# Kernel optimization log

Hardware: AMD Instinct MI355X
Metric: run time of the kernel (lower is better)

The kernel has to match this reference:

```python
import jax, jax.numpy as jnp
import numpy as np

N_NODES = 25000
N_EDGES = 250000
DIM = 64
HEADS = 4
BN_EPS = 1e-5


def setup_inputs() -> dict:
    key = jax.random.key(0)
    ks = jax.random.split(key, 6)
    x = jax.random.normal(ks[0], (N_NODES, DIM), dtype=jnp.float32)
    edge_index = jax.random.randint(ks[1], (2, N_EDGES), 0, N_NODES)
    edge_attr = jax.random.normal(ks[2], (N_EDGES, DIM), dtype=jnp.float32)
    # learned params of GATGNN_AGAT_LAYER (xavier-ish scale)
    W = jax.random.normal(ks[3], (2 * DIM, HEADS * DIM), dtype=jnp.float32) * 0.05
    att = jax.random.normal(ks[4], (1, HEADS, 2 * DIM), dtype=jnp.float32) * 0.05
    bias = jnp.zeros((DIM,), dtype=jnp.float32)
    # BatchNorm1d(heads) in eval mode (running stats)
    bn_gamma = jnp.ones((HEADS,), dtype=jnp.float32)
    bn_beta = jnp.zeros((HEADS,), dtype=jnp.float32)
    bn_mean = jnp.zeros((HEADS,), dtype=jnp.float32)
    bn_var = jnp.ones((HEADS,), dtype=jnp.float32)
    return {"x": x, "edge_attr": edge_attr, "W": W, "att": att, "bias": bias,
            "bn_gamma": bn_gamma, "bn_beta": bn_beta, "bn_mean": bn_mean,
            "bn_var": bn_var, "edge_index": edge_index}


def reference(x, edge_attr, W, att, bias, bn_gamma, bn_beta, bn_mean, bn_var, edge_index):
    act = jax.nn.softplus  # act='softplus' in DSDCrystal
    # flow='target_to_source': i = edge_index[0] (aggregation index), j = edge_index[1]
    idx_i = edge_index[0]
    idx_j = edge_index[1]
    x_i = x[idx_i]                                   # [E, D] gather
    x_j = x[idx_j]                                   # [E, D] gather
    out_i = act(jnp.concatenate([x_i, edge_attr], axis=-1) @ W)  # [E, H*D]
    out_j = act(jnp.concatenate([x_j, edge_attr], axis=-1) @ W)  # [E, H*D]
    out_i = out_i.reshape(-1, HEADS, DIM)            # [E, H, D]
    out_j = out_j.reshape(-1, HEADS, DIM)
    # multi-head attention logits
    alpha = act(jnp.sum(jnp.concatenate([out_i, out_j], axis=-1) * att, axis=-1))  # [E, H]
    # BatchNorm1d(heads), eval mode
    alpha = act((alpha - bn_mean) / jnp.sqrt(bn_var + BN_EPS) * bn_gamma + bn_beta)
    # segment softmax over edges sharing the same target node i
    amax = jax.ops.segment_max(alpha, idx_i, num_segments=N_NODES)  # [N, H]
    e = jnp.exp(alpha - amax[idx_i])
    denom = jax.ops.segment_sum(e, idx_i, num_segments=N_NODES)[idx_i]  # [E, H]
    alpha = e / denom
    # weighted messages, scatter-add aggregation (dropout p=0.0 / eval)
    msg = out_j * alpha[:, :, None]                  # [E, H, D]
    aggr = jax.ops.segment_sum(msg, idx_i, num_segments=N_NODES)  # [N, H, D]
    # update: mean over heads + bias
    return aggr.mean(axis=1) + bias                  # [N, D]
```

## Files before the change

kernel.cpp:

```cpp
#include <hip/hip_runtime.h>
#include <hip/hip_bf16.h>
#include <math.h>

#define NN 25000
#define NE 250000
#define DD 64
#define HH 4
#define NGROUP (NE / 16)

typedef __attribute__((ext_vector_type(8))) short bf16x8;
typedef __attribute__((ext_vector_type(4))) float f32x4;

#define WT_LD 136

__device__ __forceinline__ float softplus_f(float x) {
    return fmaxf(x, 0.0f) + __logf(1.0f + __expf(-fabsf(x)));
}

__device__ __forceinline__ unsigned short f2bf(float f) {
    __hip_bfloat16 h = __float2bfloat16(f);
    unsigned short u;
    __builtin_memcpy(&u, &h, 2);
    return u;
}

__device__ __forceinline__ float bf2f(unsigned short u) {
    return __uint_as_float(((unsigned int)u) << 16);
}

__device__ __forceinline__ void load8(const float* p, bf16x8& hi, bf16x8& lo) {
    float4 a = *(const float4*)p;
    float4 b = *(const float4*)(p + 4);
    float v[8] = {a.x, a.y, a.z, a.w, b.x, b.y, b.z, b.w};
#pragma unroll
    for (int i = 0; i < 8; ++i) {
        unsigned short h = f2bf(v[i]);
        hi[i] = (short)h;
        lo[i] = (short)f2bf(v[i] - bf2f(h));
    }
}

__global__ __launch_bounds__(512, 4)
void k_edge(const float* __restrict__ x, const float* __restrict__ ea,
            const float* __restrict__ W, const float* __restrict__ att,
            const float* __restrict__ bn_g, const float* __restrict__ bn_b,
            const float* __restrict__ bn_m, const float* __restrict__ bn_v,
            const int* __restrict__ eidx,
            unsigned short* __restrict__ outj,
            float* __restrict__ expa, float* __restrict__ denom)
{
    __shared__ unsigned short Wsh[256 * WT_LD];
    __shared__ float attI[256], attJ[256];

    const int tid = threadIdx.x;
    const int lane = tid & 63;
    const int q = lane >> 4;
    const int r = lane & 15;

    for (int idx = tid; idx < 32768; idx += 512) {
        int k = idx >> 8, n = idx & 255;
        Wsh[n * WT_LD + k] = f2bf(W[idx]);
    }
    if (tid < 256) {
        int c = tid;
        attI[c] = att[(c >> 6) * 128 + (c & 63)];
        attJ[c] = att[(c >> 6) * 128 + 64 + (c & 63)];
    }
    float bnsc[HH], bnsh[HH];
#pragma unroll
    for (int t = 0; t < HH; ++t) {
        float inv = rsqrtf(bn_v[t] + 1e-5f);
        bnsc[t] = bn_g[t] * inv;
        bnsh[t] = bn_b[t] - bn_m[t] * bn_g[t] * inv;
    }
    __syncthreads();

    const int gw = blockIdx.x * 8 + (tid >> 6);
    const int nw = gridDim.x * 8;

    for (int g = gw; g < NGROUP; g += nw) {
        const int e0 = g * 16;
        const int ei = eidx[e0 + r];
        const int ej = eidx[NE + e0 + r];
        const float* xi = x + (size_t)ei * DD;
        const float* xj = x + (size_t)ej * DD;
        const float* ev = ea + (size_t)(e0 + r) * DD;

        bf16x8 Ahi[6], Alo[6];
        load8(xi + q * 8,      Ahi[0], Alo[0]);
        load8(xi + 32 + q * 8, Ahi[1], Alo[1]);
        load8(xj + q * 8,      Ahi[2], Alo[2]);
        load8(xj + 32 + q * 8, Ahi[3], Alo[3]);
        load8(ev + q * 8,      Ahi[4], Alo[4]);
        load8(ev + 32 + q * 8, Ahi[5], Alo[5]);

        float lg[4][4];
#pragma unroll
        for (int a = 0; a < 4; ++a)
#pragma unroll
            for (int b = 0; b < 4; ++b) lg[a][b] = 0.f;

#pragma unroll
        for (int nt = 0; nt < 4; ++nt) {
            f32x4 ai[4], aj[4];
#pragma unroll
            for (int h = 0; h < 4; ++h) {
                ai[h] = (f32x4){0.f, 0.f, 0.f, 0.f};
                aj[h] = (f32x4){0.f, 0.f, 0.f, 0.f};
            }
#pragma unroll
            for (int h = 0; h < 4; ++h) {
                const unsigned short* bp = &Wsh[((nt + 4 * h) * 16 + r) * WT_LD + q * 8];
#pragma unroll
                for (int kt = 0; kt < 4; ++kt) {
                    bf16x8 bf = *(const bf16x8*)(bp + kt * 32);
                    const int fi = (kt < 2) ? kt : kt + 2;
                    const int fj = kt + 2;
                    ai[h] = __builtin_amdgcn_mfma_f32_16x16x32_bf16(Ahi[fi], bf, ai[h], 0, 0, 0);
                    ai[h] = __builtin_amdgcn_mfma_f32_16x16x32_bf16(Alo[fi], bf, ai[h], 0, 0, 0);
                    aj[h] = __builtin_amdgcn_mfma_f32_16x16x32_bf16(Ahi[fj], bf, aj[h], 0, 0, 0);
                    aj[h] = __builtin_amdgcn_mfma_f32_16x16x32_bf16(Alo[fj], bf, aj[h], 0, 0, 0);
                }
            }
            const int dbase = nt * 16 + r;
#pragma unroll
            for (int reg = 0; reg < 4; ++reg) {
                ushort4 pk;
                unsigned short* pkp = (unsigned short*)&pk;
#pragma unroll
                for (int h = 0; h < 4; ++h) {
                    const int c = dbase + 64 * h;
                    float spi = softplus_f(ai[h][reg]);
                    float spj = softplus_f(aj[h][reg]);
                    lg[reg][h] += spi * attI[c] + spj * attJ[c];
                    pkp[h] = f2bf(spj);
                }
                const unsigned e = (unsigned)(e0 + q * 4 + reg);
                *(ushort4*)&outj[e * 256 + dbase * 4] = pk;
            }
        }

#pragma unroll
        for (int off = 1; off < 16; off <<= 1) {
#pragma unroll
            for (int a = 0; a < 4; ++a)
#pragma unroll
                for (int b = 0; b < 4; ++b)
                    lg[a][b] += __shfl_xor(lg[a][b], off, 64);
        }
        float exv[4][4];
#pragma unroll
        for (int reg = 0; reg < 4; ++reg)
#pragma unroll
            for (int h = 0; h < 4; ++h)
                exv[reg][h] = __expf(softplus_f(fmaf(lg[reg][h], bnsc[h], bnsh[h])));

        if (r < 4) {
#pragma unroll
            for (int reg = 0; reg < 4; ++reg) {
                const int e = e0 + q * 4 + reg;
                const int ii = eidx[e];
                expa[e * 4 + r] = exv[reg][r];
                atomicAdd(&denom[ii * 4 + r], exv[reg][r]);
            }
        }
    }
}

__global__ __launch_bounds__(256)
void k_scatter(const int* __restrict__ eidx,
               const unsigned short* __restrict__ outj,
               const float* __restrict__ expa,
               const float* __restrict__ denom,
               float* __restrict__ acc)
{
    const int e = blockIdx.x * 4 + (threadIdx.x >> 6);
    const int lane = threadIdx.x & 63;
    const int i = eidx[e];
    float4 ev = *(const float4*)&expa[e * 4];
    float4 dv = *(const float4*)&denom[i * 4];
    float w0 = 0.25f * ev.x / dv.x;
    float w1 = 0.25f * ev.y / dv.y;
    float w2 = 0.25f * ev.z / dv.z;
    float w3 = 0.25f * ev.w / dv.w;
    ushort4 v = *(const ushort4*)&outj[((unsigned)e << 8) | (lane << 2)];
    float s = w0 * bf2f(v.x) + w1 * bf2f(v.y) + w2 * bf2f(v.z) + w3 * bf2f(v.w);
    atomicAdd(&acc[i * DD + lane], s);
}

__global__ __launch_bounds__(256)
void k_final(const float* __restrict__ acc, const float* __restrict__ bias,
             float* __restrict__ out)
{
    const int t = blockIdx.x * 256 + threadIdx.x;
    out[t] = acc[t] + bias[t & 63];
}

extern "C" void kernel_launch(void* const* d_in, const int* in_sizes, int n_in,
                              void* d_out, int out_size, void* d_ws, size_t ws_size,
                              hipStream_t stream)
{
    (void)in_sizes; (void)n_in; (void)out_size; (void)ws_size;
    const float* x    = (const float*)d_in[0];
    const float* ea   = (const float*)d_in[1];
    const float* W    = (const float*)d_in[2];
    const float* att  = (const float*)d_in[3];
    const float* bias = (const float*)d_in[4];
    const float* bn_g = (const float*)d_in[5];
    const float* bn_b = (const float*)d_in[6];
    const float* bn_m = (const float*)d_in[7];
    const float* bn_v = (const float*)d_in[8];
    const int*   eidx = (const int*)d_in[9];
    float* out = (float*)d_out;

    char* ws = (char*)d_ws;
    unsigned short* outj = (unsigned short*)ws;
    float* expa  = (float*)(ws + (size_t)NE * 256 * 2);
    float* denom = (float*)(ws + (size_t)NE * 256 * 2 + (size_t)NE * 16);
    float* acc   = denom + (size_t)NN * 4;

    hipMemsetAsync(denom, 0, (size_t)(NN * 4 + NN * DD) * sizeof(float), stream);

    k_edge<<<dim3(512), dim3(512), 0, stream>>>(
        x, ea, W, att, bn_g, bn_b, bn_m, bn_v, eidx, outj, expa, denom);
    k_scatter<<<dim3(NE / 4), dim3(256), 0, stream>>>(eidx, outj, expa, denom, acc);
    k_final<<<dim3((NN * DD) / 256), dim3(256), 0, stream>>>(acc, bias, out);
}
```

Before: 304.0 us.

## Replace atomic scatter with CSR-sorted per-node gather aggregation

Builds a CSR grouping of edges by target node (histogram, single-block scan, placement permutation) and replaces the atomic denominator and atomic message scatter with a per-node gather kernel. That kernel accumulates the softmax numerator and denominator in registers and writes the output directly, which also folds in the bias add. This removes 16M float atomics plus the final pass, but adds three small preprocessing kernels, including a serial single-block scan, and makes the outj reads random.

```diff
diff --git a/kernel.cpp b/kernel.cpp
--- a/kernel.cpp
+++ b/kernel.cpp
@@ -47,7 +47,7 @@
             const float* __restrict__ bn_m, const float* __restrict__ bn_v,
             const int* __restrict__ eidx,
             unsigned short* __restrict__ outj,
-            float* __restrict__ expa, float* __restrict__ denom)
+            float* __restrict__ expa)
 {
     __shared__ unsigned short Wsh[256 * WT_LD];
     __shared__ float attI[256], attJ[256];
@@ -148,52 +148,89 @@
                 for (int b = 0; b < 4; ++b)
                     lg[a][b] += __shfl_xor(lg[a][b], off, 64);
         }
-        float exv[4][4];
-#pragma unroll
-        for (int reg = 0; reg < 4; ++reg)
-#pragma unroll
-            for (int h = 0; h < 4; ++h)
-                exv[reg][h] = __expf(softplus_f(fmaf(lg[reg][h], bnsc[h], bnsh[h])));
-
         if (r < 4) {
 #pragma unroll
             for (int reg = 0; reg < 4; ++reg) {
                 const int e = e0 + q * 4 + reg;
-                const int ii = eidx[e];
-                expa[e * 4 + r] = exv[reg][r];
-                atomicAdd(&denom[ii * 4 + r], exv[reg][r]);
+                expa[e * 4 + r] = __expf(softplus_f(fmaf(lg[reg][r], bnsc[r], bnsh[r])));
             }
         }
     }
 }
 
 __global__ __launch_bounds__(256)
-void k_scatter(const int* __restrict__ eidx,
-               const unsigned short* __restrict__ outj,
-               const float* __restrict__ expa,
-               const float* __restrict__ denom,
-               float* __restrict__ acc)
+void k_hist(const int* __restrict__ eidx, int* __restrict__ cnt) {
+    const int e = blockIdx.x * 256 + threadIdx.x;
+    if (e < NE) atomicAdd(&cnt[eidx[e]], 1);
+}
+
+__global__ __launch_bounds__(1024)
+void k_scan(const int* __restrict__ cnt, int* __restrict__ offs,
+            int* __restrict__ cursor) {
+    __shared__ int sdata[1024];
+    const int tid = threadIdx.x;
+    int running = 0;
+    for (int chunk = 0; chunk < (NN + 1023) / 1024; ++chunk) {
+        const int i = chunk * 1024 + tid;
+        int v = (i < NN) ? cnt[i] : 0;
+        sdata[tid] = v;
+        __syncthreads();
+        for (int off = 1; off < 1024; off <<= 1) {
+            int t = (tid >= off) ? sdata[tid - off] : 0;
+            __syncthreads();
+            sdata[tid] += t;
+            __syncthreads();
+        }
+        if (i < NN) {
+            int excl = running + sdata[tid] - v;
+            offs[i] = excl;
+            cursor[i] = excl;
+        }
+        running += sdata[1023];
+        __syncthreads();
+    }
+    if (tid == 0) offs[NN] = NE;
+}
+
+__global__ __launch_bounds__(256)
+void k_place(const int* __restrict__ eidx, int* __restrict__ cursor,
+             int* __restrict__ perm) {
+    const int e = blockIdx.x * 256 + threadIdx.x;
+    if (e < NE) {
+        const int pos = atomicAdd(&cursor[eidx[e]], 1);
+        perm[pos] = e;
+    }
+}
+
+__global__ __launch_bounds__(256)
+void k_aggr(const int* __restrict__ offs, const int* __restrict__ perm,
+            const unsigned short* __restrict__ outj,
+            const float* __restrict__ expa,
+            const float* __restrict__ bias,
+            float* __restrict__ out)
 {
-    const int e = blockIdx.x * 4 + (threadIdx.x >> 6);
+    const int n = blockIdx.x * 4 + (threadIdx.x >> 6);
+    if (n >= NN) return;
     const int lane = threadIdx.x & 63;
-    const int i = eidx[e];
-    float4 ev = *(const float4*)&expa[e * 4];
-    float4 dv = *(const float4*)&denom[i * 4];
-    float w0 = 0.25f * ev.x / dv.x;
-    float w1 = 0.25f * ev.y / dv.y;
-    float w2 = 0.25f * ev.z / dv.z;
-    float w3 = 0.25f * ev.w / dv.w;
-    ushort4 v = *(const ushort4*)&outj[((unsigned)e << 8) | (lane << 2)];
-    float s = w0 * bf2f(v.x) + w1 * bf2f(v.y) + w2 * bf2f(v.z) + w3 * bf2f(v.w);
-    atomicAdd(&acc[i * DD + lane], s);
-}
-
-__global__ __launch_bounds__(256)
-void k_final(const float* __restrict__ acc, const float* __restrict__ bias,
-             float* __restrict__ out)
-{
-    const int t = blockIdx.x * 256 + threadIdx.x;
-    out[t] = acc[t] + bias[t & 63];
+    const int k0 = offs[n], k1 = offs[n + 1];
+    float num0 = 0.f, num1 = 0.f, num2 = 0.f, num3 = 0.f;
+    float den0 = 0.f, den1 = 0.f, den2 = 0.f, den3 = 0.f;
+    for (int k = k0; k < k1; ++k) {
+        const int e = perm[k];
+        const float4 ex = *(const float4*)&expa[e * 4];
+        const ushort4 v = *(const ushort4*)&outj[((unsigned)e << 8) | (lane << 2)];
+        num0 += ex.x * bf2f(v.x);
+        num1 += ex.y * bf2f(v.y);
+        num2 += ex.z * bf2f(v.z);
+        num3 += ex.w * bf2f(v.w);
+        den0 += ex.x; den1 += ex.y; den2 += ex.z; den3 += ex.w;
+    }
+    float r = 0.f;
+    r += (den0 > 0.f) ? num0 / den0 : 0.f;
+    r += (den1 > 0.f) ? num1 / den1 : 0.f;
+    r += (den2 > 0.f) ? num2 / den2 : 0.f;
+    r += (den3 > 0.f) ? num3 / den3 : 0.f;
+    out[n * DD + lane] = 0.25f * r + bias[lane];
 }
 
 extern "C" void kernel_launch(void* const* d_in, const int* in_sizes, int n_in,
@@ -215,14 +252,21 @@
 
     char* ws = (char*)d_ws;
     unsigned short* outj = (unsigned short*)ws;
-    float* expa  = (float*)(ws + (size_t)NE * 256 * 2);
-    float* denom = (float*)(ws + (size_t)NE * 256 * 2 + (size_t)NE * 16);
-    float* acc   = denom + (size_t)NN * 4;
-
-    hipMemsetAsync(denom, 0, (size_t)(NN * 4 + NN * DD) * sizeof(float), stream);
+    float* expa = (float*)(ws + (size_t)NE * 256 * 2);
+    int*   cnt    = (int*)(ws + (size_t)NE * 256 * 2 + (size_t)NE * 16);
+    int*   offs   = cnt + NN;
+    int*   cursor = offs + NN + 1;
+    int*   perm   = cursor + NN;
+
+    hipMemsetAsync(cnt, 0, NN * sizeof(int), stream);
+
+    k_hist <<<dim3((NE + 255) / 256), dim3(256), 0, stream>>>(eidx, cnt);
+    k_scan <<<dim3(1), dim3(1024), 0, stream>>>(cnt, offs, cursor);
+    k_place<<<dim3((NE + 255) / 256), dim3(256), 0, stream>>>(eidx, cursor, perm);
 
     k_edge<<<dim3(512), dim3(512), 0, stream>>>(
-        x, ea, W, att, bn_g, bn_b, bn_m, bn_v, eidx, outj, expa, denom);
-    k_scatter<<<dim3(NE / 4), dim3(256), 0, stream>>>(eidx, outj, expa, denom, acc);
-    k_final<<<dim3((NN * DD) / 256), dim3(256), 0, stream>>>(acc, bias, out);
-}
+        x, ea, W, att, bn_g, bn_b, bn_m, bn_v, eidx, outj, expa);
+
+    k_aggr<<<dim3((NN + 3) / 4), dim3(256), 0, stream>>>(
+        offs, perm, outj, expa, bias, out);
+}
```

New measurement: 592.8 us. 1.95x slower.
